# Kernel optimization log

Hardware: AMD Instinct MI355X
Metric: run time of the kernel (lower is better)

The kernel has to match this reference:

```python
import jax, jax.numpy as jnp
import numpy as np

NEG_BIG = -9.0e15  # matches torch's -9000000000000000.0
LEAKY_SLOPE = 0.01  # nn.LeakyReLU default


def setup_inputs() -> dict:
    key = jax.random.key(0)
    k1, k2, k3, k4, k5, k6 = jax.random.split(key, 6)
    B, N, NEMB, NHID = 1, 8192, 128, 64
    x = jax.random.normal(k1, (B, N, NEMB), dtype=jnp.float32)
    adj = jax.random.randint(k2, (B, N, N), 0, 2, dtype=jnp.int32)
    # learned parameters (xavier-ish scale)
    w_weight = jax.random.normal(k3, (NHID, NEMB), dtype=jnp.float32) * (1.0 / np.sqrt(NEMB))
    w_bias = jnp.zeros((NHID,), dtype=jnp.float32)
    a_weight = jax.random.normal(k4, (1, 2 * NHID), dtype=jnp.float32) * (1.0 / np.sqrt(2 * NHID))
    a_bias = jnp.zeros((1,), dtype=jnp.float32)
    return {"x": x, "adj": adj, "w_weight": w_weight, "w_bias": w_bias,
            "a_weight": a_weight, "a_bias": a_bias}


def reference(x, adj, w_weight, w_bias, a_weight, a_bias):
    # h = W x + b : [B, N, F]
    h = jnp.einsum("bnd,fd->bnf", x, w_weight) + w_bias
    F = h.shape[-1]
    # The torch code forms a[b,i,j] = concat(h_i, h_j) then Linear(2F->1).
    # Equivalent decomposition avoids the [B,N,N,2F] tensor:
    # e[b,i,j] = leaky_relu(h_i . a_src + h_j . a_dst + a_bias)
    a_src, a_dst = a_weight[0, :F], a_weight[0, F:]
    s_src = jnp.einsum("bnf,f->bn", h, a_src)  # [B, N]
    s_dst = jnp.einsum("bnf,f->bn", h, a_dst)  # [B, N]
    e = jax.nn.leaky_relu(s_src[:, :, None] + s_dst[:, None, :] + a_bias[0],
                          negative_slope=LEAKY_SLOPE)  # [B, N, N]
    # masked_scatter_ semantics: True positions (row-major over the WHOLE
    # flattened tensor) receive e's elements taken sequentially in order.
    mask_flat = (adj > 0).reshape(-1)
    take_idx = jnp.cumsum(mask_flat.astype(jnp.int32)) - 1  # position in source stream
    src_flat = e.reshape(-1)
    att = jnp.where(mask_flat, src_flat[take_idx], jnp.float32(NEG_BIG)).reshape(e.shape)
    # softmax over dim=2, dropout in eval mode (identity)
    att = jax.nn.softmax(att, axis=2)
    out = jax.nn.elu(jnp.einsum("bij,bjf->bif", att, h))  # [B, N, F]
    return out
```

## Files before the change

kernel.cpp:

```cpp
#include <hip/hip_runtime.h>
#include <cstdint>
#include <cstddef>

#define N 8192
#define F 64
#define NEMB 128
#define BI 16
#define BJ 256
#define NCHUNK 32
#define QCH 8
#define ROWSTR 528
#define LEAKY 0.01f

typedef __attribute__((ext_vector_type(8))) short bf16x8;
typedef __attribute__((ext_vector_type(4))) float f32x4;

__device__ __forceinline__ float wave_reduce_sum_f(float v){
  #pragma unroll
  for (int d = 32; d > 0; d >>= 1) v += __shfl_xor(v, d, 64);
  return v;
}
__device__ __forceinline__ int wave_reduce_sum_i(int v){
  #pragma unroll
  for (int d = 32; d > 0; d >>= 1) v += __shfl_xor(v, d, 64);
  return v;
}
__device__ __forceinline__ int wave_incl_scan_i(int v, int lane){
  #pragma unroll
  for (int d = 1; d < 64; d <<= 1){
    int u = __shfl_up(v, d, 64);
    if (lane >= d) v += u;
  }
  return v;
}
__device__ __forceinline__ unsigned short f2bf(float x){
  union { float f; unsigned u; } v; v.f = x;
  unsigned r = v.u + 0x7fff + ((v.u >> 16) & 1);
  return (unsigned short)(r >> 16);
}

extern "C" __global__ void __launch_bounds__(256)
k_h(const float* __restrict__ x, const float* __restrict__ ww, const float* __restrict__ wb,
    const float* __restrict__ aw, float* __restrict__ h,
    float* __restrict__ ssrc, float* __restrict__ sdst2x){
  const int t = threadIdx.x, w = t >> 6, lane = t & 63;
  __shared__ float xs[4][NEMB];
  const int n0 = blockIdx.x * 4;
  ((float2*)&xs[0][0])[t] = ((const float2*)(x + (size_t)n0 * NEMB))[t];
  __syncthreads();
  const int n = n0 + w;
  const float4* w4 = (const float4*)(ww + (size_t)lane * NEMB);
  const float4* x4 = (const float4*)&xs[w][0];
  float acc = wb[lane];
  #pragma unroll
  for (int k = 0; k < NEMB/4; ++k){
    float4 a = x4[k]; float4 b = w4[k];
    acc = fmaf(a.x, b.x, acc);
    acc = fmaf(a.y, b.y, acc);
    acc = fmaf(a.z, b.z, acc);
    acc = fmaf(a.w, b.w, acc);
  }
  h[(size_t)n * F + lane] = acc;
  float vs = wave_reduce_sum_f(acc * aw[lane]);
  float vd = wave_reduce_sum_f(acc * aw[F + lane]);
  if (lane == 0){ ssrc[n] = vs; sdst2x[n] = vd; sdst2x[n + N] = vd; }
}

extern "C" __global__ void __launch_bounds__(256)
k_tr(const float* __restrict__ h, unsigned short* __restrict__ ht){
  __shared__ float tile[64][65];
  const int t = threadIdx.x;
  const int n0 = blockIdx.x * 64;
  #pragma unroll
  for (int s = 0; s < 4; ++s){
    const int r = s*16 + (t>>4);
    const int c = (t&15)*4;
    const float4 v = *(const float4*)(h + (size_t)(n0+r)*F + c);
    tile[r][c] = v.x; tile[r][c+1] = v.y; tile[r][c+2] = v.z; tile[r][c+3] = v.w;
  }
  __syncthreads();
  const int f = t >> 2, jq = t & 3;
  unsigned short buf[16];
  #pragma unroll
  for (int k = 0; k < 16; ++k) buf[k] = f2bf(tile[jq*16 + k][f]);
  *(uint4*)(ht + (size_t)f*N + n0 + jq*16)     = *(uint4*)&buf[0];
  *(uint4*)(ht + (size_t)f*N + n0 + jq*16 + 8) = *(uint4*)&buf[8];
}

extern "C" __global__ void __launch_bounds__(256)
k_pack(const int* __restrict__ adj, unsigned short* __restrict__ bm,
       unsigned short* __restrict__ ccnt, int* __restrict__ rowtot){
  const int i = blockIdx.x, t = threadIdx.x;
  int total = 0;
  #pragma unroll
  for (int half = 0; half < 2; ++half){
    const int w = half*256 + t;
    const int4* p4 = (const int4*)(adj + (size_t)i*N + w*16);
    unsigned m = 0;
    #pragma unroll
    for (int k = 0; k < 4; ++k){
      int4 a = p4[k];
      m |= (unsigned)(a.x>0) << (k*4+0);
      m |= (unsigned)(a.y>0) << (k*4+1);
      m |= (unsigned)(a.z>0) << (k*4+2);
      m |= (unsigned)(a.w>0) << (k*4+3);
    }
    bm[((size_t)(w>>4)*N + i)*16 + (w&15)] = (unsigned short)m;
    const int pc = __popc(m);
    total += pc;
    int cs = pc;
    cs += __shfl_xor(cs, 1, 16);
    cs += __shfl_xor(cs, 2, 16);
    cs += __shfl_xor(cs, 4, 16);
    cs += __shfl_xor(cs, 8, 16);
    if ((t & 15) == 0) ccnt[(size_t)i*NCHUNK + (w>>4)] = (unsigned short)cs;
  }
  total = wave_reduce_sum_i(total);
  __shared__ int ws_[4];
  if ((t & 63) == 0) ws_[t >> 6] = total;
  __syncthreads();
  if (t == 0) rowtot[i] = ws_[0] + ws_[1] + ws_[2] + ws_[3];
}

extern "C" __global__ void __launch_bounds__(1024)
k_scan(const int* __restrict__ cnt, int* __restrict__ base){
  __shared__ int wsum[16];
  const int t = threadIdx.x, lane = t & 63, w = t >> 6;
  int4 aa = ((const int4*)cnt)[t * 2];
  int4 bb = ((const int4*)cnt)[t * 2 + 1];
  int v[8] = {aa.x, aa.y, aa.z, aa.w, bb.x, bb.y, bb.z, bb.w};
  int local = 0;
  #pragma unroll
  for (int k = 0; k < 8; ++k){ int tmp = v[k]; v[k] = local; local += tmp; }
  int inc = wave_incl_scan_i(local, lane);
  int wexcl = inc - local;
  if (lane == 63) wsum[w] = inc;
  __syncthreads();
  if (t == 0){
    int run = 0;
    #pragma unroll
    for (int k = 0; k < 16; ++k){ int tmp = wsum[k]; wsum[k] = run; run += tmp; }
  }
  __syncthreads();
  const int b0 = wsum[w] + wexcl;
  ((int4*)base)[t * 2]     = make_int4(b0 + v[0], b0 + v[1], b0 + v[2], b0 + v[3]);
  ((int4*)base)[t * 2 + 1] = make_int4(b0 + v[4], b0 + v[5], b0 + v[6], b0 + v[7]);
}

extern "C" __global__ void __launch_bounds__(256, 4)
k_main(const unsigned short* __restrict__ bm, const unsigned short* __restrict__ ccnt,
       const int* __restrict__ base, const unsigned short* __restrict__ ht,
       const float* __restrict__ ssrc, const float* __restrict__ sdst2x,
       const float* __restrict__ abias,
       float* __restrict__ pnum, float* __restrict__ pden){
  __shared__ __attribute__((aligned(16))) char pt[2][16*ROWSTR];
  __shared__ unsigned short ccum[BI][QCH];
  __shared__ int basel[BI];

  const int t = threadIdx.x, w = t >> 6, lane = t & 63;
  const int vid = blockIdx.x >> 2, quarter = blockIdx.x & 3;
  const int i0 = vid * BI;
  const int ch0 = quarter * QCH;

  if (t < BI) basel[t] = base[i0 + t];
  {
    const int r = t >> 4, g = t & 15;
    const unsigned short* cr = ccnt + (size_t)(i0+r)*NCHUNK;
    int pre = ((g < ch0) ? (int)cr[g] : 0) + ((16 + g < ch0) ? (int)cr[16 + g] : 0);
    #pragma unroll
    for (int d = 1; d < 16; d <<= 1) pre += __shfl_xor(pre, d, 16);
    int c = (g < QCH) ? (int)cr[ch0 + g] : 0;
    int inc = c;
    #pragma unroll
    for (int d = 1; d < 16; d <<= 1){ int u = __shfl_up(inc, d, 16); if (g >= d) inc += u; }
    if (g < QCH) ccum[r][g] = (unsigned short)(pre + inc - c);
  }
  __syncthreads();

  const int r = t >> 4, g = t & 15;
  const int fr = lane & 15, ks = lane >> 4;
  const int fB = w*16 + fr;
  char* buf0 = pt[0];
  char* buf1 = pt[1];
  const float ab = abias[0];
  const int rowbase = basel[r];
  float dsum = 0.f;
  f32x4 acc = {0.f, 0.f, 0.f, 0.f};
  bf16x8 bregA[8], bregB[8];

#define PREFETCH(CH, BR) { \
    const unsigned short* hBp = ht + (size_t)fB*N + (CH)*BJ + ks*8; \
    _Pragma("unroll") \
    for (int kk = 0; kk < 8; ++kk) BR[kk] = *(const bf16x8*)(hBp + kk*32); \
  }

#define PRODUCE(CC, PB) { \
    const int cc_ = (CC); \
    const int ch = ch0 + cc_; \
    const unsigned m = (unsigned)bm[((size_t)ch*N + (i0+r))*16 + g]; \
    const int c = __popc(m); \
    int inc = c; \
    _Pragma("unroll") \
    for (int d = 1; d < 16; d <<= 1){ int u = __shfl_up(inc, d, 16); if (g >= d) inc += u; } \
    const int qex = inc - c; \
    const int q0row = rowbase + (int)ccum[r][cc_]; \
    const float* sdw = sdst2x + (q0row & (N - 1)) + qex; \
    const int ilo = q0row >> 13; \
    const float s_lo = ssrc[ilo]; \
    const float s_hi = ssrc[ilo + 1]; \
    const int krel = ((ilo + 1) << 13) - q0row - qex; \
    char* myreg = (PB) + r*ROWSTR; \
    *(uint4*)(myreg + g*32)      = make_uint4(0,0,0,0); \
    *(uint4*)(myreg + g*32 + 16) = make_uint4(0,0,0,0); \
    float wv[16]; \
    _Pragma("unroll") \
    for (int k = 0; k < 16; ++k) wv[k] = sdw[k]; \
    unsigned mc = m; \
    _Pragma("unroll") \
    for (int k = 0; k < 16; ++k){ \
      const float ss = (k >= krel) ? s_hi : s_lo; \
      float e = ss + wv[k] + ab; \
      e = (e > 0.f) ? e : LEAKY * e; \
      const float p = __expf(e); \
      const int pos = __ffs(mc) - 1; \
      if (k < c){ \
        dsum += p; \
        *(unsigned short*)(myreg + g*32 + pos*2) = f2bf(p); \
      } \
      mc &= mc - 1; \
    } \
  }

#define MM(PB, BR) { \
    const char* aP = (PB) + fr*ROWSTR; \
    _Pragma("unroll") \
    for (int kk = 0; kk < 8; ++kk){ \
      bf16x8 av = *(const bf16x8*)(aP + kk*64 + ks*16); \
      acc = __builtin_amdgcn_mfma_f32_16x16x32_bf16(av, BR[kk], acc, 0, 0, 0); \
    } \
  }

  PREFETCH(ch0, bregA)
  PRODUCE(0, buf0)
  __syncthreads();
  for (int cc = 0; cc < QCH; cc += 2){
    PREFETCH(ch0 + cc + 1, bregB)
    PRODUCE(cc + 1, buf1)
    MM(buf0, bregA)
    __syncthreads();
    if (cc + 2 < QCH){
      PREFETCH(ch0 + cc + 2, bregA)
      PRODUCE(cc + 2, buf0)
    }
    MM(buf1, bregB)
    __syncthreads();
  }
#undef PREFETCH
#undef PRODUCE
#undef MM

  #pragma unroll
  for (int d = 8; d > 0; d >>= 1) dsum += __shfl_xor(dsum, d, 16);
  if (g == 0) pden[(size_t)quarter*N + i0 + r] = dsum;
  #pragma unroll
  for (int reg = 0; reg < 4; ++reg){
    const int il = ks*4 + reg;
    pnum[(size_t)quarter*N*F + (size_t)(i0 + il)*F + fB] = acc[reg];
  }
}

extern "C" __global__ void __launch_bounds__(256)
k_comb(const float* __restrict__ pnum, const float* __restrict__ pden,
       float* __restrict__ out){
  const int idx = blockIdx.x * 256 + threadIdx.x;
  const int i = idx >> 6;
  const float dn = (pden[i] + pden[N + i]) + (pden[2*N + i] + pden[3*N + i]);
  const float nm = (pnum[idx] + pnum[(size_t)N*F + idx])
                 + (pnum[2*(size_t)N*F + idx] + pnum[3*(size_t)N*F + idx]);
  float v = (dn > 0.f) ? nm / dn : 0.f;
  out[idx] = (v > 0.f) ? v : (__expf(v) - 1.f);
}

extern "C" void kernel_launch(void* const* d_in, const int* in_sizes, int n_in,
                              void* d_out, int out_size, void* d_ws, size_t ws_size,
                              hipStream_t stream){
  const float* x   = (const float*)d_in[0];
  const int*   adj = (const int*)d_in[1];
  const float* ww  = (const float*)d_in[2];
  const float* wb  = (const float*)d_in[3];
  const float* aw  = (const float*)d_in[4];
  const float* ab  = (const float*)d_in[5];
  float* out = (float*)d_out;

  char* ws = (char*)d_ws;
  float*          h      = (float*)(ws);
  unsigned short* ht     = (unsigned short*)(ws + (2u<<20));
  float*          ssrc   = (float*)(ws + (3u<<20));
  float*          sdst2x = (float*)(ws + (3u<<20) + 32*1024);
  int*            rowtot = (int*)(ws + (3u<<20) + 96*1024);
  int*            base   = (int*)(ws + (3u<<20) + 128*1024);
  unsigned short* ccnt   = (unsigned short*)(ws + (3u<<20) + 160*1024);
  unsigned short* bm     = (unsigned short*)(ws + (4u<<20));
  float*          pnum   = (float*)(ws + (12u<<20));
  float*          pden   = (float*)(ws + (20u<<20));

  k_pack<<<N,      256, 0, stream>>>(adj, bm, ccnt, rowtot);
  k_h   <<<N/4,    256, 0, stream>>>(x, ww, wb, aw, h, ssrc, sdst2x);
  k_tr  <<<N/64,   256, 0, stream>>>(h, ht);
  k_scan<<<1,     1024, 0, stream>>>(rowtot, base);
  k_main<<<4*(N/BI), 256, 0, stream>>>(bm, ccnt, base, ht, ssrc, sdst2x, ab, pnum, pden);
  k_comb<<<(N*F)/256, 256, 0, stream>>>(pnum, pden, out);
}
```

Measured before the change: 171.0 us.

## Factor exp of leaky-relu into precomputed per-node exponentials, pack bf16 stores

Precomputes exp(s_src+b), exp(0.01*(s_src+b)), exp(s_dst) and exp(0.01*s_dst) per node in k_h. The attention weight then becomes a product of two precomputed factors, with the leaky branch chosen by checking whether the product exceeds one. This removes the per-element expf from the hot PRODUCE loop. It also replaces the zero-fill plus scattered 2-byte LDS stores with bit-position iteration, where popc gives the source index, and two packed 16-byte stores. The risk is overflow or underflow of the exponentials and small rounding differences, and the per-bit popc and gather loads of float2 values could cost more than they save.

```diff
diff --git a/kernel.cpp b/kernel.cpp
--- a/kernel.cpp
+++ b/kernel.cpp
@@ -41,8 +41,8 @@
 
 extern "C" __global__ void __launch_bounds__(256)
 k_h(const float* __restrict__ x, const float* __restrict__ ww, const float* __restrict__ wb,
-    const float* __restrict__ aw, float* __restrict__ h,
-    float* __restrict__ ssrc, float* __restrict__ sdst2x){
+    const float* __restrict__ aw, const float* __restrict__ abias,
+    float* __restrict__ h, float2* __restrict__ essrc, float2* __restrict__ sdt){
   const int t = threadIdx.x, w = t >> 6, lane = t & 63;
   __shared__ float xs[4][NEMB];
   const int n0 = blockIdx.x * 4;
@@ -63,7 +63,12 @@
   h[(size_t)n * F + lane] = acc;
   float vs = wave_reduce_sum_f(acc * aw[lane]);
   float vd = wave_reduce_sum_f(acc * aw[F + lane]);
-  if (lane == 0){ ssrc[n] = vs; sdst2x[n] = vd; sdst2x[n + N] = vd; }
+  if (lane == 0){
+    const float ab = abias[0];
+    essrc[n] = make_float2(__expf(vs + ab), __expf(0.01f * (vs + ab)));
+    const float2 e2 = make_float2(__expf(vd), __expf(0.01f * vd));
+    sdt[n] = e2; sdt[n + N] = e2;
+  }
 }
 
 extern "C" __global__ void __launch_bounds__(256)
@@ -150,8 +155,7 @@
 extern "C" __global__ void __launch_bounds__(256, 4)
 k_main(const unsigned short* __restrict__ bm, const unsigned short* __restrict__ ccnt,
        const int* __restrict__ base, const unsigned short* __restrict__ ht,
-       const float* __restrict__ ssrc, const float* __restrict__ sdst2x,
-       const float* __restrict__ abias,
+       const float2* __restrict__ essrc, const float2* __restrict__ sdt,
        float* __restrict__ pnum, float* __restrict__ pden){
   __shared__ __attribute__((aligned(16))) char pt[2][16*ROWSTR];
   __shared__ unsigned short ccum[BI][QCH];
@@ -182,7 +186,6 @@
   const int fB = w*16 + fr;
   char* buf0 = pt[0];
   char* buf1 = pt[1];
-  const float ab = abias[0];
   const int rowbase = basel[r];
   float dsum = 0.f;
   f32x4 acc = {0.f, 0.f, 0.f, 0.f};
@@ -204,31 +207,28 @@
     for (int d = 1; d < 16; d <<= 1){ int u = __shfl_up(inc, d, 16); if (g >= d) inc += u; } \
     const int qex = inc - c; \
     const int q0row = rowbase + (int)ccum[r][cc_]; \
-    const float* sdw = sdst2x + (q0row & (N - 1)) + qex; \
+    const float2* sdw2 = sdt + (q0row & (N - 1)) + qex; \
     const int ilo = q0row >> 13; \
-    const float s_lo = ssrc[ilo]; \
-    const float s_hi = ssrc[ilo + 1]; \
+    const float2 Clo = essrc[ilo]; \
+    const float2 Chi = essrc[ilo + 1]; \
     const int krel = ((ilo + 1) << 13) - q0row - qex; \
-    char* myreg = (PB) + r*ROWSTR; \
-    *(uint4*)(myreg + g*32)      = make_uint4(0,0,0,0); \
-    *(uint4*)(myreg + g*32 + 16) = make_uint4(0,0,0,0); \
-    float wv[16]; \
+    unsigned pk[8]; \
     _Pragma("unroll") \
-    for (int k = 0; k < 16; ++k) wv[k] = sdw[k]; \
-    unsigned mc = m; \
-    _Pragma("unroll") \
-    for (int k = 0; k < 16; ++k){ \
-      const float ss = (k >= krel) ? s_hi : s_lo; \
-      float e = ss + wv[k] + ab; \
-      e = (e > 0.f) ? e : LEAKY * e; \
-      const float p = __expf(e); \
-      const int pos = __ffs(mc) - 1; \
-      if (k < c){ \
-        dsum += p; \
-        *(unsigned short*)(myreg + g*32 + pos*2) = f2bf(p); \
-      } \
-      mc &= mc - 1; \
+    for (int bb = 0; bb < 16; ++bb){ \
+      const int k = __popc(m & ((1u << bb) - 1u)); \
+      const float2 T = sdw2[k]; \
+      const float c1 = (k >= krel) ? Chi.x : Clo.x; \
+      const float c0 = (k >= krel) ? Chi.y : Clo.y; \
+      const float tt = c1 * T.x; \
+      float p = (tt > 1.f) ? tt : c0 * T.y; \
+      p = ((m >> bb) & 1u) ? p : 0.f; \
+      dsum += p; \
+      if (bb & 1) pk[bb >> 1] |= (unsigned)f2bf(p) << 16; \
+      else        pk[bb >> 1]  = (unsigned)f2bf(p); \
     } \
+    char* myreg = (PB) + r*ROWSTR + g*32; \
+    *(uint4*)(myreg)      = make_uint4(pk[0], pk[1], pk[2], pk[3]); \
+    *(uint4*)(myreg + 16) = make_uint4(pk[4], pk[5], pk[6], pk[7]); \
   }
 
 #define MM(PB, BR) { \
@@ -295,19 +295,19 @@
   char* ws = (char*)d_ws;
   float*          h      = (float*)(ws);
   unsigned short* ht     = (unsigned short*)(ws + (2u<<20));
-  float*          ssrc   = (float*)(ws + (3u<<20));
-  float*          sdst2x = (float*)(ws + (3u<<20) + 32*1024);
-  int*            rowtot = (int*)(ws + (3u<<20) + 96*1024);
-  int*            base   = (int*)(ws + (3u<<20) + 128*1024);
-  unsigned short* ccnt   = (unsigned short*)(ws + (3u<<20) + 160*1024);
+  float2*         essrc  = (float2*)(ws + (3u<<20));
+  float2*         sdt    = (float2*)(ws + (3u<<20) + 128*1024);
+  int*            rowtot = (int*)(ws + (3u<<20) + 256*1024);
+  int*            base   = (int*)(ws + (3u<<20) + 288*1024);
+  unsigned short* ccnt   = (unsigned short*)(ws + (3u<<20) + 320*1024);
   unsigned short* bm     = (unsigned short*)(ws + (4u<<20));
   float*          pnum   = (float*)(ws + (12u<<20));
   float*          pden   = (float*)(ws + (20u<<20));
 
   k_pack<<<N,      256, 0, stream>>>(adj, bm, ccnt, rowtot);
-  k_h   <<<N/4,    256, 0, stream>>>(x, ww, wb, aw, h, ssrc, sdst2x);
+  k_h   <<<N/4,    256, 0, stream>>>(x, ww, wb, aw, ab, h, essrc, sdt);
   k_tr  <<<N/64,   256, 0, stream>>>(h, ht);
   k_scan<<<1,     1024, 0, stream>>>(rowtot, base);
-  k_main<<<4*(N/BI), 256, 0, stream>>>(bm, ccnt, base, ht, ssrc, sdst2x, ab, pnum, pden);
+  k_main<<<4*(N/BI), 256, 0, stream>>>(bm, ccnt, base, ht, essrc, sdt, pnum, pden);
   k_comb<<<(N*F)/256, 256, 0, stream>>>(pnum, pden, out);
 }
```

Result: slower. 218.1 us (+27.6%).

## Produce attention chunks in pairs and restructure the double-buffer pipeline

Applied to the files above, without the earlier changes.

Chunk production is interleaved two at a time: both mask words, prefix scans, s_dst loads and exp/scatter loops for two chunks run together so their latencies overlap and ILP rises. The loop schedule changes from alternating produce/MMA with overlap to a phase structure: MMA both buffers, prefetch the next two B tiles, barrier, produce the next pair, barrier. This removes the overlap of production with MMA and adds register pressure from the doubled live state. The loop is fully unrolled with a switch to keep the chunk indices constant.

```diff
diff --git a/kernel.cpp b/kernel.cpp
--- a/kernel.cpp
+++ b/kernel.cpp
@@ -194,40 +194,56 @@
     for (int kk = 0; kk < 8; ++kk) BR[kk] = *(const bf16x8*)(hBp + kk*32); \
   }
 
-#define PRODUCE(CC, PB) { \
-    const int cc_ = (CC); \
-    const int ch = ch0 + cc_; \
-    const unsigned m = (unsigned)bm[((size_t)ch*N + (i0+r))*16 + g]; \
-    const int c = __popc(m); \
-    int inc = c; \
-    _Pragma("unroll") \
-    for (int d = 1; d < 16; d <<= 1){ int u = __shfl_up(inc, d, 16); if (g >= d) inc += u; } \
-    const int qex = inc - c; \
-    const int q0row = rowbase + (int)ccum[r][cc_]; \
-    const float* sdw = sdst2x + (q0row & (N - 1)) + qex; \
-    const int ilo = q0row >> 13; \
-    const float s_lo = ssrc[ilo]; \
-    const float s_hi = ssrc[ilo + 1]; \
-    const int krel = ((ilo + 1) << 13) - q0row - qex; \
-    char* myreg = (PB) + r*ROWSTR; \
-    *(uint4*)(myreg + g*32)      = make_uint4(0,0,0,0); \
-    *(uint4*)(myreg + g*32 + 16) = make_uint4(0,0,0,0); \
-    float wv[16]; \
-    _Pragma("unroll") \
-    for (int k = 0; k < 16; ++k) wv[k] = sdw[k]; \
-    unsigned mc = m; \
+#define PRODUCE_PAIR(CC0, CC1) { \
+    const int chA_ = ch0 + (CC0), chB_ = ch0 + (CC1); \
+    const unsigned mA_ = (unsigned)bm[((size_t)chA_*N + (i0+r))*16 + g]; \
+    const unsigned mB_ = (unsigned)bm[((size_t)chB_*N + (i0+r))*16 + g]; \
+    const int cA_ = __popc(mA_), cB_ = __popc(mB_); \
+    int incA_ = cA_, incB_ = cB_; \
+    _Pragma("unroll") \
+    for (int d = 1; d < 16; d <<= 1){ \
+      int uA = __shfl_up(incA_, d, 16); \
+      int uB = __shfl_up(incB_, d, 16); \
+      if (g >= d){ incA_ += uA; incB_ += uB; } \
+    } \
+    const int qexA_ = incA_ - cA_, qexB_ = incB_ - cB_; \
+    const int q0A_ = rowbase + (int)ccum[r][CC0]; \
+    const int q0B_ = rowbase + (int)ccum[r][CC1]; \
+    const float* swA_ = sdst2x + (q0A_ & (N - 1)) + qexA_; \
+    const float* swB_ = sdst2x + (q0B_ & (N - 1)) + qexB_; \
+    float wvA_[16], wvB_[16]; \
+    _Pragma("unroll") \
+    for (int k = 0; k < 16; ++k) wvA_[k] = swA_[k]; \
+    _Pragma("unroll") \
+    for (int k = 0; k < 16; ++k) wvB_[k] = swB_[k]; \
+    const int iloA_ = q0A_ >> 13, iloB_ = q0B_ >> 13; \
+    const float sloA_ = ssrc[iloA_], shiA_ = ssrc[iloA_ + 1]; \
+    const float sloB_ = ssrc[iloB_], shiB_ = ssrc[iloB_ + 1]; \
+    const int krelA_ = ((iloA_ + 1) << 13) - q0A_ - qexA_; \
+    const int krelB_ = ((iloB_ + 1) << 13) - q0B_ - qexB_; \
+    char* mr0_ = buf0 + r*ROWSTR + g*32; \
+    char* mr1_ = buf1 + r*ROWSTR + g*32; \
+    *(uint4*)(mr0_)      = make_uint4(0,0,0,0); \
+    *(uint4*)(mr0_ + 16) = make_uint4(0,0,0,0); \
+    *(uint4*)(mr1_)      = make_uint4(0,0,0,0); \
+    *(uint4*)(mr1_ + 16) = make_uint4(0,0,0,0); \
+    unsigned mcA_ = mA_, mcB_ = mB_; \
     _Pragma("unroll") \
     for (int k = 0; k < 16; ++k){ \
-      const float ss = (k >= krel) ? s_hi : s_lo; \
-      float e = ss + wv[k] + ab; \
-      e = (e > 0.f) ? e : LEAKY * e; \
-      const float p = __expf(e); \
-      const int pos = __ffs(mc) - 1; \
-      if (k < c){ \
-        dsum += p; \
-        *(unsigned short*)(myreg + g*32 + pos*2) = f2bf(p); \
-      } \
-      mc &= mc - 1; \
+      const float ssA = (k >= krelA_) ? shiA_ : sloA_; \
+      float eA = ssA + wvA_[k] + ab; \
+      eA = (eA > 0.f) ? eA : LEAKY * eA; \
+      const float pA = __expf(eA); \
+      const int posA = __ffs(mcA_) - 1; \
+      if (k < cA_){ dsum += pA; *(unsigned short*)(mr0_ + posA*2) = f2bf(pA); } \
+      mcA_ &= mcA_ - 1; \
+      const float ssB = (k >= krelB_) ? shiB_ : sloB_; \
+      float eB = ssB + wvB_[k] + ab; \
+      eB = (eB > 0.f) ? eB : LEAKY * eB; \
+      const float pB = __expf(eB); \
+      const int posB = __ffs(mcB_) - 1; \
+      if (k < cB_){ dsum += pB; *(unsigned short*)(mr1_ + posB*2) = f2bf(pB); } \
+      mcB_ &= mcB_ - 1; \
     } \
   }
 
@@ -240,23 +256,30 @@
     } \
   }
 
-  PREFETCH(ch0, bregA)
-  PRODUCE(0, buf0)
-  __syncthreads();
+  PREFETCH(ch0 + 0, bregA)
+  PREFETCH(ch0 + 1, bregB)
+  PRODUCE_PAIR(0, 1)
+  __syncthreads();
+  #pragma unroll
   for (int cc = 0; cc < QCH; cc += 2){
-    PREFETCH(ch0 + cc + 1, bregB)
-    PRODUCE(cc + 1, buf1)
     MM(buf0, bregA)
+    MM(buf1, bregB)
+    if (cc + 2 < QCH){
+      PREFETCH(ch0 + cc + 2, bregA)
+      PREFETCH(ch0 + cc + 3, bregB)
+    }
     __syncthreads();
     if (cc + 2 < QCH){
-      PREFETCH(ch0 + cc + 2, bregA)
-      PRODUCE(cc + 2, buf0)
+      switch (cc + 2){
+        case 2: PRODUCE_PAIR(2, 3) break;
+        case 4: PRODUCE_PAIR(4, 5) break;
+        default: PRODUCE_PAIR(6, 7) break;
+      }
+      __syncthreads();
     }
-    MM(buf1, bregB)
-    __syncthreads();
   }
 #undef PREFETCH
-#undef PRODUCE
+#undef PRODUCE_PAIR
 #undef MM
 
   #pragma unroll
```

Result: slower. 176.6 us (+3.3%).

## Split fused attention kernel into probability materialization and separate bf16 GEMM

Applied to the files above, without the earlier changes.

Replaces the fused produce-and-MFMA kernel with two kernels. One kernel computes masked exp probabilities per row, using an LDS window of sdst2x and popcount-based indexing, and writes a dense bf16 P matrix (128 MB). A separate MFMA GEMM then multiplies P by h^T with a 4-way K split. This removes the per-chunk prefix-count bookkeeping and the LDS double buffering, at the cost of a large extra global-memory write and read of P.

```diff
diff --git a/kernel.cpp b/kernel.cpp
--- a/kernel.cpp
+++ b/kernel.cpp
@@ -5,11 +5,6 @@
 #define N 8192
 #define F 64
 #define NEMB 128
-#define BI 16
-#define BJ 256
-#define NCHUNK 32
-#define QCH 8
-#define ROWSTR 528
 #define LEAKY 0.01f
 
 typedef __attribute__((ext_vector_type(8))) short bf16x8;
@@ -89,7 +84,7 @@
 
 extern "C" __global__ void __launch_bounds__(256)
 k_pack(const int* __restrict__ adj, unsigned short* __restrict__ bm,
-       unsigned short* __restrict__ ccnt, int* __restrict__ rowtot){
+       int* __restrict__ rowtot){
   const int i = blockIdx.x, t = threadIdx.x;
   int total = 0;
   #pragma unroll
@@ -105,15 +100,8 @@
       m |= (unsigned)(a.z>0) << (k*4+2);
       m |= (unsigned)(a.w>0) << (k*4+3);
     }
-    bm[((size_t)(w>>4)*N + i)*16 + (w&15)] = (unsigned short)m;
-    const int pc = __popc(m);
-    total += pc;
-    int cs = pc;
-    cs += __shfl_xor(cs, 1, 16);
-    cs += __shfl_xor(cs, 2, 16);
-    cs += __shfl_xor(cs, 4, 16);
-    cs += __shfl_xor(cs, 8, 16);
-    if ((t & 15) == 0) ccnt[(size_t)i*NCHUNK + (w>>4)] = (unsigned short)cs;
+    bm[(size_t)i*512 + w] = (unsigned short)m;
+    total += __popc(m);
   }
   total = wave_reduce_sum_i(total);
   __shared__ int ws_[4];
@@ -147,125 +135,116 @@
   ((int4*)base)[t * 2 + 1] = make_int4(b0 + v[4], b0 + v[5], b0 + v[6], b0 + v[7]);
 }
 
-extern "C" __global__ void __launch_bounds__(256, 4)
-k_main(const unsigned short* __restrict__ bm, const unsigned short* __restrict__ ccnt,
-       const int* __restrict__ base, const unsigned short* __restrict__ ht,
+extern "C" __global__ void __launch_bounds__(256)
+k_prod(const unsigned short* __restrict__ bm, const int* __restrict__ base,
        const float* __restrict__ ssrc, const float* __restrict__ sdst2x,
        const float* __restrict__ abias,
-       float* __restrict__ pnum, float* __restrict__ pden){
-  __shared__ __attribute__((aligned(16))) char pt[2][16*ROWSTR];
-  __shared__ unsigned short ccum[BI][QCH];
-  __shared__ int basel[BI];
-
+       unsigned short* __restrict__ P, float* __restrict__ pden){
+  __shared__ __attribute__((aligned(16))) float win[N + 32];
+  __shared__ int wtot[4];
+  __shared__ float dred[4];
   const int t = threadIdx.x, w = t >> 6, lane = t & 63;
-  const int vid = blockIdx.x >> 2, quarter = blockIdx.x & 3;
-  const int i0 = vid * BI;
-  const int ch0 = quarter * QCH;
-
-  if (t < BI) basel[t] = base[i0 + t];
-  {
-    const int r = t >> 4, g = t & 15;
-    const unsigned short* cr = ccnt + (size_t)(i0+r)*NCHUNK;
-    int pre = ((g < ch0) ? (int)cr[g] : 0) + ((16 + g < ch0) ? (int)cr[16 + g] : 0);
-    #pragma unroll
-    for (int d = 1; d < 16; d <<= 1) pre += __shfl_xor(pre, d, 16);
-    int c = (g < QCH) ? (int)cr[ch0 + g] : 0;
-    int inc = c;
-    #pragma unroll
-    for (int d = 1; d < 16; d <<= 1){ int u = __shfl_up(inc, d, 16); if (g >= d) inc += u; }
-    if (g < QCH) ccum[r][g] = (unsigned short)(pre + inc - c);
-  }
-  __syncthreads();
-
-  const int r = t >> 4, g = t & 15;
-  const int fr = lane & 15, ks = lane >> 4;
-  const int fB = w*16 + fr;
-  char* buf0 = pt[0];
-  char* buf1 = pt[1];
+  const int i = blockIdx.x;
   const float ab = abias[0];
-  const int rowbase = basel[r];
+
+  const unsigned wpair = *(const unsigned*)(bm + (size_t)i*512 + t*2);
+  const unsigned m0 = wpair & 0xffffu, m1 = wpair >> 16;
+  const int pc0 = __popc(m0), pc1 = __popc(m1);
+  const int s = pc0 + pc1;
+  const int inc = wave_incl_scan_i(s, lane);
+  if (lane == 63) wtot[w] = inc;
+  __syncthreads();
+  const int rt = wtot[0] + wtot[1] + wtot[2] + wtot[3];
+  int wexcl = 0;
+  #pragma unroll
+  for (int k = 0; k < 4; ++k) if (k < w) wexcl += wtot[k];
+  const int rel0 = wexcl + inc - s;
+  const int rel1 = rel0 + pc0;
+  const int qbase = base[i];
+  const int boff = qbase & (N - 1);
+  const int astart = boff & ~3;
+  const int shift = boff & 3;
+  const int need = shift + rt + 16;
+  for (int j = t*4; j < need; j += 1024)
+    *(float4*)&win[j] = *(const float4*)(sdst2x + astart + j);
+  __syncthreads();
+
   float dsum = 0.f;
-  f32x4 acc = {0.f, 0.f, 0.f, 0.f};
-  bf16x8 bregA[8], bregB[8];
-
-#define PREFETCH(CH, BR) { \
-    const unsigned short* hBp = ht + (size_t)fB*N + (CH)*BJ + ks*8; \
-    _Pragma("unroll") \
-    for (int kk = 0; kk < 8; ++kk) BR[kk] = *(const bf16x8*)(hBp + kk*32); \
-  }
-
-#define PRODUCE(CC, PB) { \
-    const int cc_ = (CC); \
-    const int ch = ch0 + cc_; \
-    const unsigned m = (unsigned)bm[((size_t)ch*N + (i0+r))*16 + g]; \
-    const int c = __popc(m); \
-    int inc = c; \
-    _Pragma("unroll") \
-    for (int d = 1; d < 16; d <<= 1){ int u = __shfl_up(inc, d, 16); if (g >= d) inc += u; } \
-    const int qex = inc - c; \
-    const int q0row = rowbase + (int)ccum[r][cc_]; \
-    const float* sdw = sdst2x + (q0row & (N - 1)) + qex; \
-    const int ilo = q0row >> 13; \
+  unsigned pkA[8], pkB[8];
+
+#define PRODW(M, Q, REL, PK) { \
+    const int ilo = (Q) >> 13; \
     const float s_lo = ssrc[ilo]; \
     const float s_hi = ssrc[ilo + 1]; \
-    const int krel = ((ilo + 1) << 13) - q0row - qex; \
-    char* myreg = (PB) + r*ROWSTR; \
-    *(uint4*)(myreg + g*32)      = make_uint4(0,0,0,0); \
-    *(uint4*)(myreg + g*32 + 16) = make_uint4(0,0,0,0); \
-    float wv[16]; \
+    const int krel = ((ilo + 1) << 13) - (Q); \
+    const int rbase = shift + (REL); \
     _Pragma("unroll") \
-    for (int k = 0; k < 16; ++k) wv[k] = sdw[k]; \
-    unsigned mc = m; \
-    _Pragma("unroll") \
-    for (int k = 0; k < 16; ++k){ \
+    for (int bb = 0; bb < 16; ++bb){ \
+      const int k = __popc((M) & ((1u << bb) - 1u)); \
+      const float sd = win[rbase + k]; \
       const float ss = (k >= krel) ? s_hi : s_lo; \
-      float e = ss + wv[k] + ab; \
+      float e = ss + sd + ab; \
       e = (e > 0.f) ? e : LEAKY * e; \
-      const float p = __expf(e); \
-      const int pos = __ffs(mc) - 1; \
-      if (k < c){ \
-        dsum += p; \
-        *(unsigned short*)(myreg + g*32 + pos*2) = f2bf(p); \
-      } \
-      mc &= mc - 1; \
+      float p = __expf(e); \
+      p = (((M) >> bb) & 1u) ? p : 0.f; \
+      dsum += p; \
+      if (bb & 1) (PK)[bb >> 1] |= (unsigned)f2bf(p) << 16; \
+      else        (PK)[bb >> 1]  = (unsigned)f2bf(p); \
     } \
   }
 
-#define MM(PB, BR) { \
-    const char* aP = (PB) + fr*ROWSTR; \
-    _Pragma("unroll") \
-    for (int kk = 0; kk < 8; ++kk){ \
-      bf16x8 av = *(const bf16x8*)(aP + kk*64 + ks*16); \
-      acc = __builtin_amdgcn_mfma_f32_16x16x32_bf16(av, BR[kk], acc, 0, 0, 0); \
-    } \
-  }
-
-  PREFETCH(ch0, bregA)
-  PRODUCE(0, buf0)
-  __syncthreads();
-  for (int cc = 0; cc < QCH; cc += 2){
-    PREFETCH(ch0 + cc + 1, bregB)
-    PRODUCE(cc + 1, buf1)
-    MM(buf0, bregA)
-    __syncthreads();
-    if (cc + 2 < QCH){
-      PREFETCH(ch0 + cc + 2, bregA)
-      PRODUCE(cc + 2, buf0)
-    }
-    MM(buf1, bregB)
-    __syncthreads();
-  }
-#undef PREFETCH
-#undef PRODUCE
-#undef MM
-
-  #pragma unroll
-  for (int d = 8; d > 0; d >>= 1) dsum += __shfl_xor(dsum, d, 16);
-  if (g == 0) pden[(size_t)quarter*N + i0 + r] = dsum;
+  const int q0 = qbase + rel0;
+  const int q1 = qbase + rel1;
+  PRODW(m0, q0, rel0, pkA)
+  PRODW(m1, q1, rel1, pkB)
+#undef PRODW
+
+  unsigned short* dst = P + (size_t)i*N + t*32;
+  *(uint4*)(dst)      = make_uint4(pkA[0], pkA[1], pkA[2], pkA[3]);
+  *(uint4*)(dst + 8)  = make_uint4(pkA[4], pkA[5], pkA[6], pkA[7]);
+  *(uint4*)(dst + 16) = make_uint4(pkB[0], pkB[1], pkB[2], pkB[3]);
+  *(uint4*)(dst + 24) = make_uint4(pkB[4], pkB[5], pkB[6], pkB[7]);
+
+  float ds = wave_reduce_sum_f(dsum);
+  if (lane == 0) dred[w] = ds;
+  __syncthreads();
+  if (t == 0) pden[i] = dred[0] + dred[1] + dred[2] + dred[3];
+}
+
+extern "C" __global__ void __launch_bounds__(256)
+k_gemm(const unsigned short* __restrict__ P, const unsigned short* __restrict__ ht,
+       float* __restrict__ pnum){
+  const int t = threadIdx.x, w = t >> 6, lane = t & 63;
+  const int rb = blockIdx.x >> 2, ksp = blockIdx.x & 3;
+  const int fr = lane & 15, ks = lane >> 4;
+  const int row = rb*64 + w*16 + fr;
+  const unsigned short* ap = P + (size_t)row*N + ks*8;
+  const unsigned short* b0 = ht + (size_t)(fr     )*N + ks*8;
+  const unsigned short* b1 = ht + (size_t)(fr + 16)*N + ks*8;
+  const unsigned short* b2 = ht + (size_t)(fr + 32)*N + ks*8;
+  const unsigned short* b3 = ht + (size_t)(fr + 48)*N + ks*8;
+  f32x4 a0 = {0.f,0.f,0.f,0.f}, a1 = a0, a2 = a0, a3 = a0;
+  const int koff = ksp * 2048;
+  #pragma unroll 2
+  for (int j = koff; j < koff + 2048; j += 32){
+    bf16x8 av = *(const bf16x8*)(ap + j);
+    bf16x8 v0 = *(const bf16x8*)(b0 + j);
+    bf16x8 v1 = *(const bf16x8*)(b1 + j);
+    bf16x8 v2 = *(const bf16x8*)(b2 + j);
+    bf16x8 v3 = *(const bf16x8*)(b3 + j);
+    a0 = __builtin_amdgcn_mfma_f32_16x16x32_bf16(av, v0, a0, 0, 0, 0);
+    a1 = __builtin_amdgcn_mfma_f32_16x16x32_bf16(av, v1, a1, 0, 0, 0);
+    a2 = __builtin_amdgcn_mfma_f32_16x16x32_bf16(av, v2, a2, 0, 0, 0);
+    a3 = __builtin_amdgcn_mfma_f32_16x16x32_bf16(av, v3, a3, 0, 0, 0);
+  }
+  float* outq = pnum + (size_t)ksp*N*F;
   #pragma unroll
   for (int reg = 0; reg < 4; ++reg){
-    const int il = ks*4 + reg;
-    pnum[(size_t)quarter*N*F + (size_t)(i0 + il)*F + fB] = acc[reg];
+    const int ro = rb*64 + w*16 + ks*4 + reg;
+    outq[(size_t)ro*F + fr     ] = a0[reg];
+    outq[(size_t)ro*F + fr + 16] = a1[reg];
+    outq[(size_t)ro*F + fr + 32] = a2[reg];
+    outq[(size_t)ro*F + fr + 48] = a3[reg];
   }
 }
 
@@ -274,7 +253,7 @@
        float* __restrict__ out){
   const int idx = blockIdx.x * 256 + threadIdx.x;
   const int i = idx >> 6;
-  const float dn = (pden[i] + pden[N + i]) + (pden[2*N + i] + pden[3*N + i]);
+  const float dn = pden[i];
   const float nm = (pnum[idx] + pnum[(size_t)N*F + idx])
                  + (pnum[2*(size_t)N*F + idx] + pnum[3*(size_t)N*F + idx]);
   float v = (dn > 0.f) ? nm / dn : 0.f;
@@ -296,18 +275,19 @@
   float*          h      = (float*)(ws);
   unsigned short* ht     = (unsigned short*)(ws + (2u<<20));
   float*          ssrc   = (float*)(ws + (3u<<20));
-  float*          sdst2x = (float*)(ws + (3u<<20) + 32*1024);
-  int*            rowtot = (int*)(ws + (3u<<20) + 96*1024);
-  int*            base   = (int*)(ws + (3u<<20) + 128*1024);
-  unsigned short* ccnt   = (unsigned short*)(ws + (3u<<20) + 160*1024);
+  float*          sdst2x = (float*)(ws + (3u<<20) + 64*1024);
+  int*            rowtot = (int*)(ws + (3u<<20) + 256*1024);
+  int*            base   = (int*)(ws + (3u<<20) + 288*1024);
   unsigned short* bm     = (unsigned short*)(ws + (4u<<20));
-  float*          pnum   = (float*)(ws + (12u<<20));
-  float*          pden   = (float*)(ws + (20u<<20));
-
-  k_pack<<<N,      256, 0, stream>>>(adj, bm, ccnt, rowtot);
-  k_h   <<<N/4,    256, 0, stream>>>(x, ww, wb, aw, h, ssrc, sdst2x);
-  k_tr  <<<N/64,   256, 0, stream>>>(h, ht);
-  k_scan<<<1,     1024, 0, stream>>>(rowtot, base);
-  k_main<<<4*(N/BI), 256, 0, stream>>>(bm, ccnt, base, ht, ssrc, sdst2x, ab, pnum, pden);
+  unsigned short* P      = (unsigned short*)(ws + (16u<<20));
+  float*          pnum   = (float*)(ws + (144u<<20));
+  float*          pden   = (float*)(ws + (152u<<20));
+
+  k_pack<<<N,    256, 0, stream>>>(adj, bm, rowtot);
+  k_h   <<<N/4,  256, 0, stream>>>(x, ww, wb, aw, h, ssrc, sdst2x);
+  k_tr  <<<N/64, 256, 0, stream>>>(h, ht);
+  k_scan<<<1,   1024, 0, stream>>>(rowtot, base);
+  k_prod<<<N,    256, 0, stream>>>(bm, base, ssrc, sdst2x, ab, P, pden);
+  k_gemm<<<512,  256, 0, stream>>>(P, ht, pnum);
   k_comb<<<(N*F)/256, 256, 0, stream>>>(pnum, pden, out);
 }
```

After: 222.7 us. +30.3%, slower.
